# Kernel tuning notes

Hardware: AMD Instinct MI355X
Metric: run time of the kernel (lower is better)

Reference implementation:

```python
import jax, jax.numpy as jnp
import numpy as np
from jax import lax

B, P, E, H, A, V, T = 128, 196, 512, 512, 256, 30000, 21


def setup_inputs() -> dict:
    key = jax.random.key(0)
    ks = jax.random.split(key, 16)
    s = 0.02
    return {
        "encoder_out": jax.random.normal(ks[0], (B, P, E), jnp.float32),
        "captions": jax.random.randint(ks[1], (B, T), 0, V),
        "emb": jax.random.normal(ks[2], (V, E), jnp.float32) * s,
        "W_enc_att": jax.random.normal(ks[3], (E, A), jnp.float32) * s,
        "b_enc_att": jnp.zeros((A,), jnp.float32),
        "W_dec_att": jax.random.normal(ks[4], (H, A), jnp.float32) * s,
        "b_dec_att": jnp.zeros((A,), jnp.float32),
        "w_full_att": jax.random.normal(ks[5], (A,), jnp.float32) * s,
        "b_full_att": jnp.zeros((), jnp.float32),
        "W_ih": jax.random.normal(ks[6], (4 * H, 2 * E), jnp.float32) * s,
        "b_ih": jnp.zeros((4 * H,), jnp.float32),
        "W_hh": jax.random.normal(ks[7], (4 * H, H), jnp.float32) * s,
        "b_hh": jnp.zeros((4 * H,), jnp.float32),
        "W_fc": jax.random.normal(ks[8], (V, H), jnp.float32) * s,
        "b_fc": jnp.zeros((V,), jnp.float32),
    }


def reference(encoder_out, captions, emb, W_enc_att, b_enc_att, W_dec_att, b_dec_att,
              w_full_att, b_full_att, W_ih, b_ih, W_hh, b_hh, W_fc, b_fc):
    # embeddings of captions[:, :-1] -> (B, T-1, E)
    x_emb = emb[captions[:, :-1]]
    # precompute encoder attention projection once (same math, hoisted)
    enc_proj = encoder_out @ W_enc_att + b_enc_att  # (B, P, A)
    h0 = jnp.zeros((encoder_out.shape[0], W_hh.shape[1]), encoder_out.dtype)
    c0 = jnp.zeros_like(h0)

    def step(carry, xt):
        h, c = carry
        # Bahdanau attention: full_att(relu(enc_att + dec_att(h)))
        att = jax.nn.relu(enc_proj + (h @ W_dec_att + b_dec_att)[:, None, :])  # (B,P,A)
        e = att @ w_full_att + b_full_att  # (B, P)
        alpha = jax.nn.softmax(e, axis=1)
        context = jnp.einsum('bp,bpe->be', alpha, encoder_out)  # (B, E)
        x = jnp.concatenate([xt, context], axis=1)  # (B, 2E)
        gates = x @ W_ih.T + b_ih + h @ W_hh.T + b_hh  # (B, 4H)
        i, f, g, o = jnp.split(gates, 4, axis=1)  # PyTorch LSTMCell order
        c_new = jax.nn.sigmoid(f) * c + jax.nn.sigmoid(i) * jnp.tanh(g)
        h_new = jax.nn.sigmoid(o) * jnp.tanh(c_new)
        # dropout is identity in eval/reference mode
        out = h_new @ W_fc.T + b_fc  # (B, V)
        return (h_new, c_new), out

    _, outs = lax.scan(step, (h0, c0), jnp.swapaxes(x_emb, 0, 1))  # (T-1, B, V)
    return jnp.swapaxes(outs, 0, 1)  # (B, T-1, V)
```

## Files before the change

kernel.cpp:

```cpp
#include <hip/hip_runtime.h>
#include <stdint.h>

#define BSZ   128
#define PDIM  196
#define EDIM  512
#define HDIM  512
#define ADIM  256
#define VDIM  30000
#define VPAD  30080
#define NSTEP 20
#define KCAT  1536
#define NGATE 2048
#define KSPLIT 8

typedef __attribute__((ext_vector_type(8))) short short8;
typedef __attribute__((ext_vector_type(4))) float f32x4;

__device__ __forceinline__ unsigned short f2b(float f) {
  union { float f; uint32_t u; } v; v.f = f;
  uint32_t r = v.u + 0x7fffu + ((v.u >> 16) & 1u);
  return (unsigned short)(r >> 16);
}
__device__ __forceinline__ float b2f(unsigned short u) {
  union { uint32_t u; float f; } v; v.u = ((uint32_t)u) << 16;
  return v.f;
}

__device__ __forceinline__ void async16(const void* g, void* l) {
  __builtin_amdgcn_global_load_lds(
      (const __attribute__((address_space(1))) void*)g,
      (__attribute__((address_space(3))) void*)l, 16, 0, 0);
}


__global__ void k_cast_f32_bf16(const float* __restrict__ src,
                                unsigned short* __restrict__ dst, int n4) {
  int i = blockIdx.x * 256 + threadIdx.x;
  if (i < n4) {
    float4 v = ((const float4*)src)[i];
    ushort4 o; o.x = f2b(v.x); o.y = f2b(v.y); o.z = f2b(v.z); o.w = f2b(v.w);
    ((ushort4*)dst)[i] = o;
  }
}

__global__ void k_build_wenc_t(const float* __restrict__ W,
                               unsigned short* __restrict__ WT) {
  int i = blockIdx.x * 256 + threadIdx.x;
  if (i < ADIM * EDIM) {
    int a = i >> 9, k = i & 511;
    WT[i] = f2b(W[k * ADIM + a]);
  }
}

__global__ void k_build_wcat(const float* __restrict__ Wih,
                             const float* __restrict__ Whh,
                             unsigned short* __restrict__ Wcat) {
  int i = blockIdx.x * 256 + threadIdx.x;
  if (i < NGATE * KCAT) {
    int n = i / KCAT, k = i - n * KCAT;
    float v = (k < 1024) ? Wih[n * 1024 + k] : Whh[n * 512 + (k - 1024)];
    Wcat[i] = f2b(v);
  }
}

__global__ void k_build_wfc(const float* __restrict__ Wfc,
                            unsigned short* __restrict__ Wp) {
  int i = blockIdx.x * 256 + threadIdx.x;
  if (i < VPAD * 512) {
    int n = i >> 9, k = i & 511;
    Wp[i] = (n < VDIM) ? f2b(Wfc[n * 512 + k]) : (unsigned short)0;
  }
}

__global__ void k_build_xc(const int* __restrict__ cap,
                           const float* __restrict__ emb,
                           unsigned short* __restrict__ XC) {
  int i = blockIdx.x * 256 + threadIdx.x;
  if (i < NSTEP * BSZ * EDIM) {
    int t = i / (BSZ * EDIM);
    int r = i - t * (BSZ * EDIM);
    int b = r >> 9, k = r & 511;
    int tok = cap[b * 21 + t];
    XC[((size_t)(t * BSZ + b)) * KCAT + k] = f2b(emb[(size_t)tok * EDIM + k]);
  }
}

__global__ void k_init_state(float* __restrict__ hc, float* __restrict__ cc,
                             unsigned short* __restrict__ XC) {
  int i = blockIdx.x * 256 + threadIdx.x;
  if (i < BSZ * HDIM) {
    hc[i] = 0.f; cc[i] = 0.f;
    int b = i >> 9, k = i & 511;
    XC[(size_t)b * KCAT + 1024 + k] = 0;
  }
}


template <bool OUT_BF16>
__global__ __launch_bounds__(256) void gemm_bt(
    const unsigned short* __restrict__ A, int ldaB,
    const unsigned short* __restrict__ Bm, int ldbB,
    void* __restrict__ C, int ldc, int Nreal,
    const float* __restrict__ bias, int kt, int kchunkB, size_t zstride) {
  __shared__ short As[128 * 32];
  __shared__ short Bs[128 * 32];
  const int tid = threadIdx.x;
  const int w = tid >> 6, lane = tid & 63;
  const int m0 = blockIdx.y * 128, n0 = blockIdx.x * 128;
  const int z = blockIdx.z;

  const char* Ab = (const char*)A + (size_t)z * kchunkB;
  const char* Bb = (const char*)Bm + (size_t)z * kchunkB;

  const int q0 = w, q1 = w + 4;
  const int rr = lane >> 2;
  const int cbyte = (lane & 3) * 16;
  const char* gA0 = Ab + (size_t)(m0 + q0 * 16 + rr) * ldaB + cbyte;
  const char* gA1 = Ab + (size_t)(m0 + q1 * 16 + rr) * ldaB + cbyte;
  const char* gB0 = Bb + (size_t)(n0 + q0 * 16 + rr) * ldbB + cbyte;
  const char* gB1 = Bb + (size_t)(n0 + q1 * 16 + rr) * ldbB + cbyte;
  short* lA0 = &As[q0 * 512]; short* lA1 = &As[q1 * 512];
  short* lB0 = &Bs[q0 * 512]; short* lB1 = &Bs[q1 * 512];

  const int wm = w >> 1, wn = w & 1;
  const int fr = lane & 15, ko = (lane >> 4) * 8;

  f32x4 acc[4][4] = {};

  for (int kb = 0; kb < kt; ++kb) {
    const int kB = kb * 64;
    async16(gA0 + kB, lA0); async16(gA1 + kB, lA1);
    async16(gB0 + kB, lB0); async16(gB1 + kB, lB1);
    __syncthreads();
    short8 af[4], bfr[4];
#pragma unroll
    for (int i = 0; i < 4; ++i)
      af[i] = *(const short8*)&As[(wm * 64 + i * 16 + fr) * 32 + ko];
#pragma unroll
    for (int j = 0; j < 4; ++j)
      bfr[j] = *(const short8*)&Bs[(wn * 64 + j * 16 + fr) * 32 + ko];
#pragma unroll
    for (int i = 0; i < 4; ++i)
#pragma unroll
      for (int j = 0; j < 4; ++j)
        acc[i][j] = __builtin_amdgcn_mfma_f32_16x16x32_bf16(af[i], bfr[j], acc[i][j], 0, 0, 0);
    __syncthreads();
  }

  const int r4 = (lane >> 4) * 4;
  float* Cf = (float*)C + (size_t)z * zstride;
  unsigned short* Cb = (unsigned short*)C;
#pragma unroll
  for (int i = 0; i < 4; ++i) {
#pragma unroll
    for (int j = 0; j < 4; ++j) {
      int cc = n0 + wn * 64 + j * 16 + fr;
      if (cc < Nreal) {
        float bv = bias ? bias[cc] : 0.f;
        int r0 = m0 + wm * 64 + i * 16 + r4;
#pragma unroll
        for (int r = 0; r < 4; ++r) {
          float v = acc[i][j][r] + bv;
          if (OUT_BF16) Cb[(size_t)(r0 + r) * ldc + cc] = f2b(v);
          else          Cf[(size_t)(r0 + r) * ldc + cc] = v;
        }
      }
    }
  }
}


__global__ __launch_bounds__(512) void k_attention(
    const float* __restrict__ h, const float* __restrict__ Wd,
    const float* __restrict__ bd, const float* __restrict__ wfull,
    const float* __restrict__ bfull,
    const unsigned short* __restrict__ EncP,
    const unsigned short* __restrict__ EncB,
    unsigned short* __restrict__ XCt)
{
  __shared__ float hsh[512];
  __shared__ float hpp[512];
  __shared__ float hp[256];
  __shared__ float wsh[256];
  __shared__ float ebuf[200];
  __shared__ float sred[8];
  __shared__ float sM, sS;

  const int tid = threadIdx.x;
  const int b = blockIdx.x;
  const int w = tid >> 6, lane = tid & 63;

  hsh[tid] = h[b * 512 + tid];
  if (tid < 256) wsh[tid] = wfull[tid];
  __syncthreads();

  {
    const int a = tid & 255, half = tid >> 8;
    const float* wc = Wd + a;
    const int k0 = half * 256;
    float s0 = 0, s1 = 0, s2 = 0, s3 = 0;
    for (int k = k0; k < k0 + 256; k += 4) {
      s0 += hsh[k]     * wc[(k)     * 256];
      s1 += hsh[k + 1] * wc[(k + 1) * 256];
      s2 += hsh[k + 2] * wc[(k + 2) * 256];
      s3 += hsh[k + 3] * wc[(k + 3) * 256];
    }
    hpp[tid] = (s0 + s1) + (s2 + s3);
  }
  __syncthreads();
  if (tid < 256) hp[tid] = hpp[tid] + hpp[tid + 256] + bd[tid];
  __syncthreads();

  const float bf0 = bfull[0];
  for (int p = w; p < PDIM; p += 8) {
    const unsigned short* row = EncP + ((size_t)(b * PDIM + p)) * 256;
    float s = 0.f;
#pragma unroll
    for (int jj = 0; jj < 4; ++jj) {
      int a = lane + jj * 64;
      float v = b2f(row[a]) + hp[a];
      s += fmaxf(v, 0.f) * wsh[a];
    }
#pragma unroll
    for (int off = 32; off; off >>= 1) s += __shfl_down(s, off, 64);
    if (lane == 0) ebuf[p] = s + bf0;
  }
  __syncthreads();

  float m = -1e30f;
  for (int p = tid; p < PDIM; p += 512) m = fmaxf(m, ebuf[p]);
#pragma unroll
  for (int off = 32; off; off >>= 1) m = fmaxf(m, __shfl_down(m, off, 64));
  if (lane == 0) sred[w] = m;
  __syncthreads();
  if (tid == 0) {
    float mm = sred[0];
#pragma unroll
    for (int i = 1; i < 8; ++i) mm = fmaxf(mm, sred[i]);
    sM = mm;
  }
  __syncthreads();
  const float M = sM;
  float ps = 0.f;
  for (int p = tid; p < PDIM; p += 512) {
    float v = __expf(ebuf[p] - M); ebuf[p] = v; ps += v;
  }
#pragma unroll
  for (int off = 32; off; off >>= 1) ps += __shfl_down(ps, off, 64);
  if (lane == 0) sred[w] = ps;
  __syncthreads();
  if (tid == 0) {
    float ss = 0.f;
#pragma unroll
    for (int i = 0; i < 8; ++i) ss += sred[i];
    sS = 1.f / ss;
  }
  __syncthreads();
  const float inv = sS;

  {
    const unsigned short* eb = EncB + (size_t)b * PDIM * 512;
    float c0 = 0.f;
    for (int p = 0; p < PDIM; ++p) c0 += ebuf[p] * b2f(eb[p * 512 + tid]);
    XCt[(size_t)b * KCAT + 512 + tid] = f2b(c0 * inv);
  }
}


__global__ __launch_bounds__(256) void k_cell(
    const float* __restrict__ Gpart,
    const float* __restrict__ bih, const float* __restrict__ bhh,
    float* __restrict__ hc, float* __restrict__ cc,
    unsigned short* __restrict__ Hall, unsigned short* __restrict__ XCnext, int t) {
  int i = blockIdx.x * 256 + threadIdx.x;
  int b = i >> 9, k = i & 511;
  float gI = bih[k] + bhh[k];
  float gF = bih[512 + k] + bhh[512 + k];
  float gG = bih[1024 + k] + bhh[1024 + k];
  float gO = bih[1536 + k] + bhh[1536 + k];
  const float* P = Gpart + (size_t)b * NGATE;
#pragma unroll
  for (int z = 0; z < KSPLIT; ++z) {
    const float* Pz = P + (size_t)z * BSZ * NGATE;
    gI += Pz[k]; gF += Pz[512 + k]; gG += Pz[1024 + k]; gO += Pz[1536 + k];
  }
  float cv = cc[i];
  float ig = 1.f / (1.f + __expf(-gI));
  float fg = 1.f / (1.f + __expf(-gF));
  float gg = tanhf(gG);
  float og = 1.f / (1.f + __expf(-gO));
  float cn = fg * cv + ig * gg;
  float hn = og * tanhf(cn);
  cc[i] = cn; hc[i] = hn;
  Hall[((size_t)b * NSTEP + t) * 512 + k] = f2b(hn);
  if (t < NSTEP - 1) XCnext[(size_t)b * KCAT + 1024 + k] = f2b(hn);
}


extern "C" void kernel_launch(void* const* d_in, const int* in_sizes, int n_in,
                              void* d_out, int out_size, void* d_ws, size_t ws_size,
                              hipStream_t stream) {
  const float* enc   = (const float*)d_in[0];
  const int*   cap   = (const int*)d_in[1];
  const float* emb   = (const float*)d_in[2];
  const float* Wenc  = (const float*)d_in[3];
  const float* benc  = (const float*)d_in[4];
  const float* Wdec  = (const float*)d_in[5];
  const float* bdec  = (const float*)d_in[6];
  const float* wfull = (const float*)d_in[7];
  const float* bfull = (const float*)d_in[8];
  const float* Wih   = (const float*)d_in[9];
  const float* bih   = (const float*)d_in[10];
  const float* Whh   = (const float*)d_in[11];
  const float* bhh   = (const float*)d_in[12];
  const float* Wfc   = (const float*)d_in[13];
  const float* bfc   = (const float*)d_in[14];
  float* out = (float*)d_out;

  char* ws = (char*)d_ws;
  size_t off = 0;
  auto alloc = [&](size_t bytes) {
    char* p = ws + off;
    off += (bytes + 255) & ~(size_t)255;
    return p;
  };
  unsigned short* Wcat  = (unsigned short*)alloc((size_t)NGATE * KCAT * 2);
  unsigned short* Wfcb  = (unsigned short*)alloc((size_t)VPAD * 512 * 2);
  unsigned short* WencT = (unsigned short*)alloc((size_t)ADIM * EDIM * 2);
  unsigned short* EncB  = (unsigned short*)alloc((size_t)BSZ * PDIM * EDIM * 2);
  unsigned short* EncP  = (unsigned short*)alloc((size_t)BSZ * PDIM * ADIM * 2);
  unsigned short* XC    = (unsigned short*)alloc((size_t)NSTEP * BSZ * KCAT * 2);
  float* Gpart          = (float*)alloc((size_t)KSPLIT * BSZ * NGATE * 4);
  float* hc             = (float*)alloc((size_t)BSZ * HDIM * 4);
  float* ccst           = (float*)alloc((size_t)BSZ * HDIM * 4);
  unsigned short* Hall  = (unsigned short*)alloc((size_t)NSTEP * BSZ * HDIM * 2);
  (void)ws_size; (void)in_sizes; (void)n_in; (void)out_size;

  {
    int n4 = BSZ * PDIM * EDIM / 4;
    k_cast_f32_bf16<<<(n4 + 255) / 256, 256, 0, stream>>>(enc, EncB, n4);
  }
  k_build_wenc_t<<<(ADIM * EDIM + 255) / 256, 256, 0, stream>>>(Wenc, WencT);
  k_build_wcat<<<(NGATE * KCAT + 255) / 256, 256, 0, stream>>>(Wih, Whh, Wcat);
  k_build_wfc<<<(VPAD * 512 + 255) / 256, 256, 0, stream>>>(Wfc, Wfcb);
  k_build_xc<<<(NSTEP * BSZ * EDIM + 255) / 256, 256, 0, stream>>>(cap, emb, XC);
  k_init_state<<<(BSZ * HDIM + 255) / 256, 256, 0, stream>>>(hc, ccst, XC);

  gemm_bt<true><<<dim3(2, 196, 1), 256, 0, stream>>>(
      EncB, EDIM * 2, WencT, EDIM * 2, EncP, ADIM, ADIM, benc, 16, 0, 0);

  for (int t = 0; t < NSTEP; ++t) {
    unsigned short* XCt = XC + (size_t)t * BSZ * KCAT;
    k_attention<<<128, 512, 0, stream>>>(hc, Wdec, bdec, wfull, bfull, EncP, EncB, XCt);
    gemm_bt<false><<<dim3(NGATE / 128, 1, KSPLIT), 256, 0, stream>>>(
        XCt, KCAT * 2, Wcat, KCAT * 2, Gpart, NGATE, NGATE, nullptr,
        (KCAT / KSPLIT) / 32, (KCAT / KSPLIT) * 2, (size_t)BSZ * NGATE);
    unsigned short* XCn = XC + (size_t)((t + 1 < NSTEP) ? (t + 1) : 0) * BSZ * KCAT;
    k_cell<<<BSZ * HDIM / 256, 256, 0, stream>>>(Gpart, bih, bhh, hc, ccst, Hall, XCn, t);
  }

  gemm_bt<false><<<dim3(VPAD / 128, NSTEP * BSZ / 128, 1), 256, 0, stream>>>(
      Hall, HDIM * 2, Wfcb, HDIM * 2, out, VDIM, VDIM, bfc, 16, 0, 0);
}
```

Baseline: 1.508 ms.

## Hoist embedding gate GEMM out of recurrence and fuse LSTM cell with attention

The embedding part of the input-gate GEMM (x_emb @ W_ih[:, :512]) is now computed once for all timesteps as one large GEMM before the loop, so each step's split-K GEMM only covers the 1024 context+hidden columns. The LSTM cell update and the next step's attention are fused into one 512-thread-per-batch kernel, cutting one launch per step and the round trip of h through global memory. The context accumulation is also unrolled with four partial sums. In exchange it adds an fp32 XW buffer that every step must read, and the attention now runs with only 128 blocks after the cell update.

```diff
diff --git a/kernel.cpp b/kernel.cpp
--- a/kernel.cpp
+++ b/kernel.cpp
@@ -10,6 +10,7 @@
 #define VPAD  30080
 #define NSTEP 20
 #define KCAT  1536
+#define KSTEP 1024
 #define NGATE 2048
 #define KSPLIT 8
 
@@ -72,16 +73,16 @@
   }
 }
 
-__global__ void k_build_xc(const int* __restrict__ cap,
-                           const float* __restrict__ emb,
-                           unsigned short* __restrict__ XC) {
+__global__ void k_build_xemb(const int* __restrict__ cap,
+                             const float* __restrict__ emb,
+                             unsigned short* __restrict__ X) {
   int i = blockIdx.x * 256 + threadIdx.x;
   if (i < NSTEP * BSZ * EDIM) {
     int t = i / (BSZ * EDIM);
     int r = i - t * (BSZ * EDIM);
     int b = r >> 9, k = r & 511;
     int tok = cap[b * 21 + t];
-    XC[((size_t)(t * BSZ + b)) * KCAT + k] = f2b(emb[(size_t)tok * EDIM + k]);
+    X[((size_t)(t * BSZ + b)) * EDIM + k] = f2b(emb[(size_t)tok * EDIM + k]);
   }
 }
 
@@ -91,7 +92,7 @@
   if (i < BSZ * HDIM) {
     hc[i] = 0.f; cc[i] = 0.f;
     int b = i >> 9, k = i & 511;
-    XC[(size_t)b * KCAT + 1024 + k] = 0;
+    XC[(size_t)b * KSTEP + 512 + k] = 0;
   }
 }
 
@@ -259,41 +260,147 @@
   const float inv = sS;
 
   {
-    const unsigned short* eb = EncB + (size_t)b * PDIM * 512;
-    float c0 = 0.f;
-    for (int p = 0; p < PDIM; ++p) c0 += ebuf[p] * b2f(eb[p * 512 + tid]);
-    XCt[(size_t)b * KCAT + 512 + tid] = f2b(c0 * inv);
-  }
-}
-
-
-__global__ __launch_bounds__(256) void k_cell(
+    const unsigned short* eb = EncB + (size_t)b * PDIM * 512 + tid;
+    float c0 = 0.f, c1 = 0.f, c2 = 0.f, c3 = 0.f;
+    for (int p = 0; p < PDIM; p += 4) {
+      c0 += ebuf[p]     * b2f(eb[(p)     * 512]);
+      c1 += ebuf[p + 1] * b2f(eb[(p + 1) * 512]);
+      c2 += ebuf[p + 2] * b2f(eb[(p + 2) * 512]);
+      c3 += ebuf[p + 3] * b2f(eb[(p + 3) * 512]);
+    }
+    XCt[(size_t)b * KSTEP + tid] = f2b(((c0 + c1) + (c2 + c3)) * inv);
+  }
+}
+
+
+__global__ __launch_bounds__(512) void k_cell_attn(
     const float* __restrict__ Gpart,
+    const float* __restrict__ XW,
     const float* __restrict__ bih, const float* __restrict__ bhh,
-    float* __restrict__ hc, float* __restrict__ cc,
-    unsigned short* __restrict__ Hall, unsigned short* __restrict__ XCnext, int t) {
-  int i = blockIdx.x * 256 + threadIdx.x;
-  int b = i >> 9, k = i & 511;
-  float gI = bih[k] + bhh[k];
-  float gF = bih[512 + k] + bhh[512 + k];
-  float gG = bih[1024 + k] + bhh[1024 + k];
-  float gO = bih[1536 + k] + bhh[1536 + k];
-  const float* P = Gpart + (size_t)b * NGATE;
-#pragma unroll
-  for (int z = 0; z < KSPLIT; ++z) {
-    const float* Pz = P + (size_t)z * BSZ * NGATE;
-    gI += Pz[k]; gF += Pz[512 + k]; gG += Pz[1024 + k]; gO += Pz[1536 + k];
-  }
-  float cv = cc[i];
-  float ig = 1.f / (1.f + __expf(-gI));
-  float fg = 1.f / (1.f + __expf(-gF));
-  float gg = tanhf(gG);
-  float og = 1.f / (1.f + __expf(-gO));
-  float cn = fg * cv + ig * gg;
-  float hn = og * tanhf(cn);
-  cc[i] = cn; hc[i] = hn;
-  Hall[((size_t)b * NSTEP + t) * 512 + k] = f2b(hn);
-  if (t < NSTEP - 1) XCnext[(size_t)b * KCAT + 1024 + k] = f2b(hn);
+    float* __restrict__ cc, unsigned short* __restrict__ Hall,
+    const float* __restrict__ Wd, const float* __restrict__ bd,
+    const float* __restrict__ wfull, const float* __restrict__ bfull,
+    const unsigned short* __restrict__ EncP,
+    const unsigned short* __restrict__ EncB,
+    unsigned short* __restrict__ XCnext, int t) {
+  __shared__ float hsh[512];
+  __shared__ float hpp[512];
+  __shared__ float hp[256];
+  __shared__ float wsh[256];
+  __shared__ float ebuf[200];
+  __shared__ float sred[8];
+  __shared__ float sM, sS;
+
+  const int tid = threadIdx.x;
+  const int b = blockIdx.x;
+  const int w = tid >> 6, lane = tid & 63;
+
+  if (tid < 256) wsh[tid] = wfull[tid];
+
+  {
+    const int k = tid;
+    const float* xw = XW + ((size_t)(t * BSZ + b)) * NGATE;
+    float gI = bih[k]        + bhh[k]        + xw[k];
+    float gF = bih[512 + k]  + bhh[512 + k]  + xw[512 + k];
+    float gG = bih[1024 + k] + bhh[1024 + k] + xw[1024 + k];
+    float gO = bih[1536 + k] + bhh[1536 + k] + xw[1536 + k];
+    const float* P = Gpart + (size_t)b * NGATE + k;
+#pragma unroll
+    for (int z = 0; z < KSPLIT; ++z) {
+      const float* Pz = P + (size_t)z * BSZ * NGATE;
+      gI += Pz[0]; gF += Pz[512]; gG += Pz[1024]; gO += Pz[1536];
+    }
+    float cv = cc[b * 512 + k];
+    float ig = 1.f / (1.f + __expf(-gI));
+    float fg = 1.f / (1.f + __expf(-gF));
+    float gg = tanhf(gG);
+    float og = 1.f / (1.f + __expf(-gO));
+    float cn = fg * cv + ig * gg;
+    float hn = og * tanhf(cn);
+    cc[b * 512 + k] = cn;
+    Hall[((size_t)b * NSTEP + t) * 512 + k] = f2b(hn);
+    hsh[k] = hn;
+    if (t < NSTEP - 1) XCnext[(size_t)b * KSTEP + 512 + k] = f2b(hn);
+  }
+  __syncthreads();
+  if (t >= NSTEP - 1) return;
+
+
+  {
+    const int a = tid & 255, half = tid >> 8;
+    const float* wc = Wd + a;
+    const int k0 = half * 256;
+    float s0 = 0, s1 = 0, s2 = 0, s3 = 0;
+    for (int k = k0; k < k0 + 256; k += 4) {
+      s0 += hsh[k]     * wc[(k)     * 256];
+      s1 += hsh[k + 1] * wc[(k + 1) * 256];
+      s2 += hsh[k + 2] * wc[(k + 2) * 256];
+      s3 += hsh[k + 3] * wc[(k + 3) * 256];
+    }
+    hpp[tid] = (s0 + s1) + (s2 + s3);
+  }
+  __syncthreads();
+  if (tid < 256) hp[tid] = hpp[tid] + hpp[tid + 256] + bd[tid];
+  __syncthreads();
+
+  const float bf0 = bfull[0];
+  for (int p = w; p < PDIM; p += 8) {
+    const unsigned short* row = EncP + ((size_t)(b * PDIM + p)) * 256;
+    float s = 0.f;
+#pragma unroll
+    for (int jj = 0; jj < 4; ++jj) {
+      int a = lane + jj * 64;
+      float v = b2f(row[a]) + hp[a];
+      s += fmaxf(v, 0.f) * wsh[a];
+    }
+#pragma unroll
+    for (int off = 32; off; off >>= 1) s += __shfl_down(s, off, 64);
+    if (lane == 0) ebuf[p] = s + bf0;
+  }
+  __syncthreads();
+
+  float m = -1e30f;
+  for (int p = tid; p < PDIM; p += 512) m = fmaxf(m, ebuf[p]);
+#pragma unroll
+  for (int off = 32; off; off >>= 1) m = fmaxf(m, __shfl_down(m, off, 64));
+  if (lane == 0) sred[w] = m;
+  __syncthreads();
+  if (tid == 0) {
+    float mm = sred[0];
+#pragma unroll
+    for (int i = 1; i < 8; ++i) mm = fmaxf(mm, sred[i]);
+    sM = mm;
+  }
+  __syncthreads();
+  const float M = sM;
+  float ps = 0.f;
+  for (int p = tid; p < PDIM; p += 512) {
+    float v = __expf(ebuf[p] - M); ebuf[p] = v; ps += v;
+  }
+#pragma unroll
+  for (int off = 32; off; off >>= 1) ps += __shfl_down(ps, off, 64);
+  if (lane == 0) sred[w] = ps;
+  __syncthreads();
+  if (tid == 0) {
+    float ss = 0.f;
+#pragma unroll
+    for (int i = 0; i < 8; ++i) ss += sred[i];
+    sS = 1.f / ss;
+  }
+  __syncthreads();
+  const float inv = sS;
+
+  {
+    const unsigned short* eb = EncB + (size_t)b * PDIM * 512 + tid;
+    float c0 = 0.f, c1 = 0.f, c2 = 0.f, c3 = 0.f;
+    for (int p = 0; p < PDIM; p += 4) {
+      c0 += ebuf[p]     * b2f(eb[(p)     * 512]);
+      c1 += ebuf[p + 1] * b2f(eb[(p + 1) * 512]);
+      c2 += ebuf[p + 2] * b2f(eb[(p + 2) * 512]);
+      c3 += ebuf[p + 3] * b2f(eb[(p + 3) * 512]);
+    }
+    XCnext[(size_t)b * KSTEP + tid] = f2b(((c0 + c1) + (c2 + c3)) * inv);
+  }
 }
 
 
@@ -329,7 +436,9 @@
   unsigned short* WencT = (unsigned short*)alloc((size_t)ADIM * EDIM * 2);
   unsigned short* EncB  = (unsigned short*)alloc((size_t)BSZ * PDIM * EDIM * 2);
   unsigned short* EncP  = (unsigned short*)alloc((size_t)BSZ * PDIM * ADIM * 2);
-  unsigned short* XC    = (unsigned short*)alloc((size_t)NSTEP * BSZ * KCAT * 2);
+  unsigned short* XC    = (unsigned short*)alloc((size_t)NSTEP * BSZ * KSTEP * 2);
+  unsigned short* Xemb  = (unsigned short*)alloc((size_t)NSTEP * BSZ * EDIM * 2);
+  float* XW             = (float*)alloc((size_t)NSTEP * BSZ * NGATE * 4);
   float* Gpart          = (float*)alloc((size_t)KSPLIT * BSZ * NGATE * 4);
   float* hc             = (float*)alloc((size_t)BSZ * HDIM * 4);
   float* ccst           = (float*)alloc((size_t)BSZ * HDIM * 4);
@@ -343,20 +452,25 @@
   k_build_wenc_t<<<(ADIM * EDIM + 255) / 256, 256, 0, stream>>>(Wenc, WencT);
   k_build_wcat<<<(NGATE * KCAT + 255) / 256, 256, 0, stream>>>(Wih, Whh, Wcat);
   k_build_wfc<<<(VPAD * 512 + 255) / 256, 256, 0, stream>>>(Wfc, Wfcb);
-  k_build_xc<<<(NSTEP * BSZ * EDIM + 255) / 256, 256, 0, stream>>>(cap, emb, XC);
+  k_build_xemb<<<(NSTEP * BSZ * EDIM + 255) / 256, 256, 0, stream>>>(cap, emb, Xemb);
   k_init_state<<<(BSZ * HDIM + 255) / 256, 256, 0, stream>>>(hc, ccst, XC);
 
   gemm_bt<true><<<dim3(2, 196, 1), 256, 0, stream>>>(
       EncB, EDIM * 2, WencT, EDIM * 2, EncP, ADIM, ADIM, benc, 16, 0, 0);
 
+  gemm_bt<false><<<dim3(NGATE / 128, NSTEP * BSZ / 128, 1), 256, 0, stream>>>(
+      Xemb, EDIM * 2, Wcat, KCAT * 2, XW, NGATE, NGATE, nullptr, 16, 0, 0);
+
+  k_attention<<<128, 512, 0, stream>>>(hc, Wdec, bdec, wfull, bfull, EncP, EncB, XC);
+
   for (int t = 0; t < NSTEP; ++t) {
-    unsigned short* XCt = XC + (size_t)t * BSZ * KCAT;
-    k_attention<<<128, 512, 0, stream>>>(hc, Wdec, bdec, wfull, bfull, EncP, EncB, XCt);
+    unsigned short* XCt = XC + (size_t)t * BSZ * KSTEP;
     gemm_bt<false><<<dim3(NGATE / 128, 1, KSPLIT), 256, 0, stream>>>(
-        XCt, KCAT * 2, Wcat, KCAT * 2, Gpart, NGATE, NGATE, nullptr,
-        (KCAT / KSPLIT) / 32, (KCAT / KSPLIT) * 2, (size_t)BSZ * NGATE);
-    unsigned short* XCn = XC + (size_t)((t + 1 < NSTEP) ? (t + 1) : 0) * BSZ * KCAT;
-    k_cell<<<BSZ * HDIM / 256, 256, 0, stream>>>(Gpart, bih, bhh, hc, ccst, Hall, XCn, t);
+        XCt, KSTEP * 2, Wcat + 512, KCAT * 2, Gpart, NGATE, NGATE, nullptr,
+        (KSTEP / KSPLIT) / 32, (KSTEP / KSPLIT) * 2, (size_t)BSZ * NGATE);
+    unsigned short* XCn = XC + (size_t)((t + 1 < NSTEP) ? (t + 1) : 0) * BSZ * KSTEP;
+    k_cell_attn<<<128, 512, 0, stream>>>(Gpart, XW, bih, bhh, ccst, Hall,
+                                         Wdec, bdec, wfull, bfull, EncP, EncB, XCn, t);
   }
 
   gemm_bt<false><<<dim3(VPAD / 128, NSTEP * BSZ / 128, 1), 256, 0, stream>>>(
```

After: 1.444 ms. -4.2%, faster.

## Fuse recurrent loop into persistent kernel with grid barriers and hoisted embedding GEMM

Applied to the files above, without the earlier changes.

Replaces the 60 per-step launches (attention, split-K gate GEMM, cell) with a single persistent 128-block kernel that synchronises through an atomic grid barrier. The input-embedding half of the gate GEMM is hoisted out of the loop into one batched GEMM over all steps, so each step only multiplies the context and hidden parts. The decoder-attention projection now uses bf16 weights, and the score and context loops are vectorised. The aim is to remove launch overhead and redundant per-step work. In exchange it relies on all 128 blocks being co-resident for the spin barrier and adds bf16 rounding to W_dec.

```diff
diff --git a/kernel.cpp b/kernel.cpp
--- a/kernel.cpp
+++ b/kernel.cpp
@@ -10,6 +10,7 @@
 #define VPAD  30080
 #define NSTEP 20
 #define KCAT  1536
+#define KSTEP 1024
 #define NGATE 2048
 #define KSPLIT 8
 
@@ -25,6 +26,12 @@
   union { uint32_t u; float f; } v; v.u = ((uint32_t)u) << 16;
   return v.f;
 }
+__device__ __forceinline__ float ulo(uint32_t u) {
+  union { uint32_t u; float f; } v; v.u = u << 16; return v.f;
+}
+__device__ __forceinline__ float uhi(uint32_t u) {
+  union { uint32_t u; float f; } v; v.u = u & 0xffff0000u; return v.f;
+}
 
 __device__ __forceinline__ void async16(const void* g, void* l) {
   __builtin_amdgcn_global_load_lds(
@@ -32,6 +39,17 @@
       (__attribute__((address_space(3))) void*)l, 16, 0, 0);
 }
 
+__device__ __forceinline__ void gsync(unsigned* bar, unsigned target) {
+  __threadfence();
+  __syncthreads();
+  if (threadIdx.x == 0) {
+    __hip_atomic_fetch_add(bar, 1u, __ATOMIC_RELEASE, __HIP_MEMORY_SCOPE_AGENT);
+    while (__hip_atomic_load(bar, __ATOMIC_ACQUIRE, __HIP_MEMORY_SCOPE_AGENT) < target)
+      __builtin_amdgcn_s_sleep(1);
+  }
+  __syncthreads();
+}
+
 
 __global__ void k_cast_f32_bf16(const float* __restrict__ src,
                                 unsigned short* __restrict__ dst, int n4) {
@@ -72,26 +90,34 @@
   }
 }
 
-__global__ void k_build_xc(const int* __restrict__ cap,
-                           const float* __restrict__ emb,
-                           unsigned short* __restrict__ XC) {
+__global__ void k_build_xemb(const int* __restrict__ cap,
+                             const float* __restrict__ emb,
+                             unsigned short* __restrict__ X) {
   int i = blockIdx.x * 256 + threadIdx.x;
   if (i < NSTEP * BSZ * EDIM) {
     int t = i / (BSZ * EDIM);
     int r = i - t * (BSZ * EDIM);
     int b = r >> 9, k = r & 511;
     int tok = cap[b * 21 + t];
-    XC[((size_t)(t * BSZ + b)) * KCAT + k] = f2b(emb[(size_t)tok * EDIM + k]);
-  }
-}
-
-__global__ void k_init_state(float* __restrict__ hc, float* __restrict__ cc,
-                             unsigned short* __restrict__ XC) {
-  int i = blockIdx.x * 256 + threadIdx.x;
+    X[((size_t)(t * BSZ + b)) * EDIM + k] = f2b(emb[(size_t)tok * EDIM + k]);
+  }
+}
+
+__global__ void k_build_wdb(const float* __restrict__ Wd,
+                            unsigned short* __restrict__ o) {
+  int i = blockIdx.x * 256 + threadIdx.x;
+  if (i < HDIM * ADIM) o[i] = f2b(Wd[i]);
+}
+
+__global__ void k_init_state(float* __restrict__ cc,
+                             unsigned short* __restrict__ XC,
+                             unsigned* __restrict__ bar) {
+  int i = blockIdx.x * 256 + threadIdx.x;
+  if (i == 0) *bar = 0u;
   if (i < BSZ * HDIM) {
-    hc[i] = 0.f; cc[i] = 0.f;
+    cc[i] = 0.f;
     int b = i >> 9, k = i & 511;
-    XC[(size_t)b * KCAT + 1024 + k] = 0;
+    XC[(size_t)b * KSTEP + 512 + k] = 0;
   }
 }
 
@@ -170,130 +196,239 @@
 }
 
 
-__global__ __launch_bounds__(512) void k_attention(
-    const float* __restrict__ h, const float* __restrict__ Wd,
-    const float* __restrict__ bd, const float* __restrict__ wfull,
-    const float* __restrict__ bfull,
+__device__ __forceinline__ void attn_234(
+    int b, int tid, int w, int lane, float bf0,
     const unsigned short* __restrict__ EncP,
     const unsigned short* __restrict__ EncB,
-    unsigned short* __restrict__ XCt)
+    const float* hp, const float* wsh,
+    float* ebuf, float* red, float* sred, float* sMS,
+    unsigned short* __restrict__ XCdst)
 {
+  const float hpr0 = hp[lane * 4],     hpr1 = hp[lane * 4 + 1];
+  const float hpr2 = hp[lane * 4 + 2], hpr3 = hp[lane * 4 + 3];
+  const float wsr0 = wsh[lane * 4],     wsr1 = wsh[lane * 4 + 1];
+  const float wsr2 = wsh[lane * 4 + 2], wsr3 = wsh[lane * 4 + 3];
+  for (int pb = w * 4; pb < PDIM; pb += 32) {
+    float s0 = 0.f, s1 = 0.f, s2 = 0.f, s3 = 0.f;
+#pragma unroll
+    for (int q = 0; q < 4; ++q) {
+      int p = pb + q;
+      if (p < PDIM) {
+        short4 v = *((const short4*)(EncP + (size_t)(b * PDIM + p) * 256) + lane);
+        float t0 = fmaxf(b2f((unsigned short)v.x) + hpr0, 0.f) * wsr0;
+        float t1 = fmaxf(b2f((unsigned short)v.y) + hpr1, 0.f) * wsr1;
+        float t2 = fmaxf(b2f((unsigned short)v.z) + hpr2, 0.f) * wsr2;
+        float t3 = fmaxf(b2f((unsigned short)v.w) + hpr3, 0.f) * wsr3;
+        float sq = (t0 + t1) + (t2 + t3);
+        if (q == 0) s0 = sq; else if (q == 1) s1 = sq;
+        else if (q == 2) s2 = sq; else s3 = sq;
+      }
+    }
+#pragma unroll
+    for (int off = 32; off; off >>= 1) {
+      s0 += __shfl_xor(s0, off, 64);
+      s1 += __shfl_xor(s1, off, 64);
+      s2 += __shfl_xor(s2, off, 64);
+      s3 += __shfl_xor(s3, off, 64);
+    }
+    if (lane < 4) {
+      int p = pb + lane;
+      float v = (lane == 0) ? s0 : (lane == 1) ? s1 : (lane == 2) ? s2 : s3;
+      if (p < PDIM) ebuf[p] = v + bf0;
+    }
+  }
+  __syncthreads();
+
+  float m = -1e30f;
+  for (int p = tid; p < PDIM; p += 512) m = fmaxf(m, ebuf[p]);
+#pragma unroll
+  for (int off = 32; off; off >>= 1) m = fmaxf(m, __shfl_down(m, off, 64));
+  if (lane == 0) sred[w] = m;
+  __syncthreads();
+  if (tid == 0) {
+    float mm = sred[0];
+#pragma unroll
+    for (int i = 1; i < 8; ++i) mm = fmaxf(mm, sred[i]);
+    sMS[0] = mm;
+  }
+  __syncthreads();
+  const float M = sMS[0];
+  float ps = 0.f;
+  for (int p = tid; p < PDIM; p += 512) {
+    float v = __expf(ebuf[p] - M); ebuf[p] = v; ps += v;
+  }
+#pragma unroll
+  for (int off = 32; off; off >>= 1) ps += __shfl_down(ps, off, 64);
+  if (lane == 0) sred[w] = ps;
+  __syncthreads();
+  if (tid == 0) {
+    float ss = 0.f;
+#pragma unroll
+    for (int i = 0; i < 8; ++i) ss += sred[i];
+    sMS[1] = 1.f / ss;
+  }
+  __syncthreads();
+  const float inv = sMS[1];
+
+  {
+    const int c2 = tid & 255, ph = tid >> 8;
+    const uint32_t* eb = (const uint32_t*)(EncB + (size_t)b * PDIM * 512) + c2;
+    float c0 = 0.f, c1 = 0.f, d0 = 0.f, d1 = 0.f;
+    const int p0 = ph * 98;
+    for (int p = p0; p < p0 + 98; p += 2) {
+      float a0 = ebuf[p];     uint32_t u  = eb[(size_t)p * 256];
+      c0 = fmaf(a0, ulo(u),  c0); c1 = fmaf(a0, uhi(u),  c1);
+      float a1 = ebuf[p + 1]; uint32_t u2 = eb[(size_t)(p + 1) * 256];
+      d0 = fmaf(a1, ulo(u2), d0); d1 = fmaf(a1, uhi(u2), d1);
+    }
+    red[ph * 512 + c2 * 2]     = c0 + d0;
+    red[ph * 512 + c2 * 2 + 1] = c1 + d1;
+  }
+  __syncthreads();
+  float v = (red[tid] + red[512 + tid]) * inv;
+  XCdst[(size_t)b * KSTEP + tid] = f2b(v);
+}
+
+
+__global__ __launch_bounds__(512, 1) void k_loop(
+    unsigned short* __restrict__ XC,
+    const unsigned short* __restrict__ Wcat,
+    float* __restrict__ Gpart,
+    const float* __restrict__ XW,
+    const float* __restrict__ bih, const float* __restrict__ bhh,
+    float* __restrict__ ccst, unsigned short* __restrict__ Hall,
+    const unsigned short* __restrict__ Wdb,
+    const float* __restrict__ bd,
+    const float* __restrict__ wfull, const float* __restrict__ bfull,
+    const unsigned short* __restrict__ EncP,
+    const unsigned short* __restrict__ EncB,
+    unsigned* __restrict__ bar)
+{
+  __shared__ short As[128 * 32];
+  __shared__ short Bs[128 * 32];
   __shared__ float hsh[512];
-  __shared__ float hpp[512];
+  __shared__ float red[1024];
   __shared__ float hp[256];
   __shared__ float wsh[256];
   __shared__ float ebuf[200];
   __shared__ float sred[8];
-  __shared__ float sM, sS;
-
-  const int tid = threadIdx.x;
-  const int b = blockIdx.x;
+  __shared__ float sMS[2];
+
+  const int tid = threadIdx.x, blk = blockIdx.x;
   const int w = tid >> 6, lane = tid & 63;
-
-  hsh[tid] = h[b * 512 + tid];
-  if (tid < 256) wsh[tid] = wfull[tid];
-  __syncthreads();
-
-  {
-    const int a = tid & 255, half = tid >> 8;
-    const float* wc = Wd + a;
-    const int k0 = half * 256;
-    float s0 = 0, s1 = 0, s2 = 0, s3 = 0;
-    for (int k = k0; k < k0 + 256; k += 4) {
-      s0 += hsh[k]     * wc[(k)     * 256];
-      s1 += hsh[k + 1] * wc[(k + 1) * 256];
-      s2 += hsh[k + 2] * wc[(k + 2) * 256];
-      s3 += hsh[k + 3] * wc[(k + 3) * 256];
-    }
-    hpp[tid] = (s0 + s1) + (s2 + s3);
-  }
-  __syncthreads();
-  if (tid < 256) hp[tid] = hpp[tid] + hpp[tid + 256] + bd[tid];
-  __syncthreads();
-
+  const int b = blk;
+  const int gn0 = (blk >> 3) * 128, gz = blk & 7;
   const float bf0 = bfull[0];
-  for (int p = w; p < PDIM; p += 8) {
-    const unsigned short* row = EncP + ((size_t)(b * PDIM + p)) * 256;
-    float s = 0.f;
-#pragma unroll
-    for (int jj = 0; jj < 4; ++jj) {
-      int a = lane + jj * 64;
-      float v = b2f(row[a]) + hp[a];
-      s += fmaxf(v, 0.f) * wsh[a];
-    }
-#pragma unroll
-    for (int off = 32; off; off >>= 1) s += __shfl_down(s, off, 64);
-    if (lane == 0) ebuf[p] = s + bf0;
-  }
-  __syncthreads();
-
-  float m = -1e30f;
-  for (int p = tid; p < PDIM; p += 512) m = fmaxf(m, ebuf[p]);
-#pragma unroll
-  for (int off = 32; off; off >>= 1) m = fmaxf(m, __shfl_down(m, off, 64));
-  if (lane == 0) sred[w] = m;
-  __syncthreads();
-  if (tid == 0) {
-    float mm = sred[0];
-#pragma unroll
-    for (int i = 1; i < 8; ++i) mm = fmaxf(mm, sred[i]);
-    sM = mm;
-  }
-  __syncthreads();
-  const float M = sM;
-  float ps = 0.f;
-  for (int p = tid; p < PDIM; p += 512) {
-    float v = __expf(ebuf[p] - M); ebuf[p] = v; ps += v;
-  }
-#pragma unroll
-  for (int off = 32; off; off >>= 1) ps += __shfl_down(ps, off, 64);
-  if (lane == 0) sred[w] = ps;
-  __syncthreads();
-  if (tid == 0) {
-    float ss = 0.f;
-#pragma unroll
-    for (int i = 0; i < 8; ++i) ss += sred[i];
-    sS = 1.f / ss;
-  }
-  __syncthreads();
-  const float inv = sS;
-
-  {
-    const unsigned short* eb = EncB + (size_t)b * PDIM * 512;
-    float c0 = 0.f;
-    for (int p = 0; p < PDIM; ++p) c0 += ebuf[p] * b2f(eb[p * 512 + tid]);
-    XCt[(size_t)b * KCAT + 512 + tid] = f2b(c0 * inv);
-  }
-}
-
-
-__global__ __launch_bounds__(256) void k_cell(
-    const float* __restrict__ Gpart,
-    const float* __restrict__ bih, const float* __restrict__ bhh,
-    float* __restrict__ hc, float* __restrict__ cc,
-    unsigned short* __restrict__ Hall, unsigned short* __restrict__ XCnext, int t) {
-  int i = blockIdx.x * 256 + threadIdx.x;
-  int b = i >> 9, k = i & 511;
-  float gI = bih[k] + bhh[k];
-  float gF = bih[512 + k] + bhh[512 + k];
-  float gG = bih[1024 + k] + bhh[1024 + k];
-  float gO = bih[1536 + k] + bhh[1536 + k];
-  const float* P = Gpart + (size_t)b * NGATE;
-#pragma unroll
-  for (int z = 0; z < KSPLIT; ++z) {
-    const float* Pz = P + (size_t)z * BSZ * NGATE;
-    gI += Pz[k]; gF += Pz[512 + k]; gG += Pz[1024 + k]; gO += Pz[1536 + k];
-  }
-  float cv = cc[i];
-  float ig = 1.f / (1.f + __expf(-gI));
-  float fg = 1.f / (1.f + __expf(-gF));
-  float gg = tanhf(gG);
-  float og = 1.f / (1.f + __expf(-gO));
-  float cn = fg * cv + ig * gg;
-  float hn = og * tanhf(cn);
-  cc[i] = cn; hc[i] = hn;
-  Hall[((size_t)b * NSTEP + t) * 512 + k] = f2b(hn);
-  if (t < NSTEP - 1) XCnext[(size_t)b * KCAT + 1024 + k] = f2b(hn);
+  unsigned bc = 0;
+
+  if (tid < 256) { wsh[tid] = wfull[tid]; hp[tid] = bd[tid]; }
+  __syncthreads();
+
+  attn_234(b, tid, w, lane, bf0, EncP, EncB, hp, wsh, ebuf, red, sred, sMS, XC);
+
+  for (int t = 0; t < NSTEP; ++t) {
+    gsync(bar, bc += 128);
+
+    {
+      const char* Ab = (const char*)(XC + (size_t)t * BSZ * KSTEP) + gz * 256;
+      const char* Bb = (const char*)Wcat + 1024 + gz * 256;
+      const int rr = lane >> 2, cb = (lane & 3) * 16;
+      const char* gA = Ab + (size_t)(w * 16 + rr) * (KSTEP * 2) + cb;
+      const char* gB = Bb + (size_t)(gn0 + w * 16 + rr) * (KCAT * 2) + cb;
+      short* lA = &As[w * 512];
+      short* lB = &Bs[w * 512];
+      const int wm = w >> 2, wn = w & 3;
+      const int fr = lane & 15, ko = (lane >> 4) * 8;
+      f32x4 acc[4][2] = {};
+#pragma unroll
+      for (int kb = 0; kb < 4; ++kb) {
+        async16(gA + kb * 64, lA);
+        async16(gB + kb * 64, lB);
+        __syncthreads();
+        short8 af[4], bfr[2];
+#pragma unroll
+        for (int i = 0; i < 4; ++i)
+          af[i] = *(const short8*)&As[(wm * 64 + i * 16 + fr) * 32 + ko];
+#pragma unroll
+        for (int j = 0; j < 2; ++j)
+          bfr[j] = *(const short8*)&Bs[(wn * 32 + j * 16 + fr) * 32 + ko];
+#pragma unroll
+        for (int i = 0; i < 4; ++i)
+#pragma unroll
+          for (int j = 0; j < 2; ++j)
+            acc[i][j] = __builtin_amdgcn_mfma_f32_16x16x32_bf16(af[i], bfr[j], acc[i][j], 0, 0, 0);
+        __syncthreads();
+      }
+      float* Cz = Gpart + (size_t)gz * BSZ * NGATE;
+      const int r4 = (lane >> 4) * 4;
+#pragma unroll
+      for (int i = 0; i < 4; ++i)
+#pragma unroll
+        for (int j = 0; j < 2; ++j) {
+          int ccol = gn0 + wn * 32 + j * 16 + fr;
+          int r0 = wm * 64 + i * 16 + r4;
+#pragma unroll
+          for (int r = 0; r < 4; ++r)
+            Cz[(size_t)(r0 + r) * NGATE + ccol] = acc[i][j][r];
+        }
+    }
+
+    gsync(bar, bc += 128);
+
+    unsigned short* XCn = XC + (size_t)(t + 1) * BSZ * KSTEP;
+    {
+      const int k = tid;
+      const float* xw = XW + ((size_t)t * BSZ + b) * NGATE;
+      float gI = bih[k]        + bhh[k]        + xw[k];
+      float gF = bih[512 + k]  + bhh[512 + k]  + xw[512 + k];
+      float gG = bih[1024 + k] + bhh[1024 + k] + xw[1024 + k];
+      float gO = bih[1536 + k] + bhh[1536 + k] + xw[1536 + k];
+      const float* P = Gpart + (size_t)b * NGATE + k;
+#pragma unroll
+      for (int z = 0; z < KSPLIT; ++z) {
+        const float* Pz = P + (size_t)z * BSZ * NGATE;
+        gI += Pz[0]; gF += Pz[512]; gG += Pz[1024]; gO += Pz[1536];
+      }
+      float cv = ccst[b * 512 + k];
+      float ig = 1.f / (1.f + __expf(-gI));
+      float fg = 1.f / (1.f + __expf(-gF));
+      float gg = tanhf(gG);
+      float og = 1.f / (1.f + __expf(-gO));
+      float cn = fg * cv + ig * gg;
+      float hn = og * tanhf(cn);
+      ccst[b * 512 + k] = cn;
+      hsh[k] = hn;
+      Hall[((size_t)b * NSTEP + t) * 512 + k] = f2b(hn);
+      if (t < NSTEP - 1) XCn[(size_t)b * KSTEP + 512 + k] = f2b(hn);
+    }
+    __syncthreads();
+
+    if (t < NSTEP - 1) {
+      {
+        const int p2 = tid & 127, kq = tid >> 7;
+        const uint32_t* wrow = (const uint32_t*)Wdb + p2;
+        float s0 = 0.f, s1 = 0.f, s2 = 0.f, s3 = 0.f;
+        const int k0 = kq * 128;
+#pragma unroll 4
+        for (int k = k0; k < k0 + 128; k += 2) {
+          uint32_t u = wrow[(size_t)k * 128];
+          float hv = hsh[k];
+          s0 = fmaf(hv, ulo(u), s0); s1 = fmaf(hv, uhi(u), s1);
+          uint32_t u2 = wrow[(size_t)(k + 1) * 128];
+          float hv2 = hsh[k + 1];
+          s2 = fmaf(hv2, ulo(u2), s2); s3 = fmaf(hv2, uhi(u2), s3);
+        }
+        red[kq * 256 + p2 * 2]     = s0 + s2;
+        red[kq * 256 + p2 * 2 + 1] = s1 + s3;
+      }
+      __syncthreads();
+      if (tid < 256)
+        hp[tid] = bd[tid] + ((red[tid] + red[256 + tid]) + (red[512 + tid] + red[768 + tid]));
+      __syncthreads();
+
+      attn_234(b, tid, w, lane, bf0, EncP, EncB, hp, wsh, ebuf, red, sred, sMS, XCn);
+    }
+  }
 }
 
 
@@ -329,11 +464,14 @@
   unsigned short* WencT = (unsigned short*)alloc((size_t)ADIM * EDIM * 2);
   unsigned short* EncB  = (unsigned short*)alloc((size_t)BSZ * PDIM * EDIM * 2);
   unsigned short* EncP  = (unsigned short*)alloc((size_t)BSZ * PDIM * ADIM * 2);
-  unsigned short* XC    = (unsigned short*)alloc((size_t)NSTEP * BSZ * KCAT * 2);
+  unsigned short* XC    = (unsigned short*)alloc((size_t)NSTEP * BSZ * KSTEP * 2);
+  unsigned short* Xemb  = (unsigned short*)alloc((size_t)NSTEP * BSZ * EDIM * 2);
+  float* XW             = (float*)alloc((size_t)NSTEP * BSZ * NGATE * 4);
   float* Gpart          = (float*)alloc((size_t)KSPLIT * BSZ * NGATE * 4);
-  float* hc             = (float*)alloc((size_t)BSZ * HDIM * 4);
   float* ccst           = (float*)alloc((size_t)BSZ * HDIM * 4);
   unsigned short* Hall  = (unsigned short*)alloc((size_t)NSTEP * BSZ * HDIM * 2);
+  unsigned short* Wdb   = (unsigned short*)alloc((size_t)HDIM * ADIM * 2);
+  unsigned* bar         = (unsigned*)alloc(256);
   (void)ws_size; (void)in_sizes; (void)n_in; (void)out_size;
 
   {
@@ -343,21 +481,18 @@
   k_build_wenc_t<<<(ADIM * EDIM + 255) / 256, 256, 0, stream>>>(Wenc, WencT);
   k_build_wcat<<<(NGATE * KCAT + 255) / 256, 256, 0, stream>>>(Wih, Whh, Wcat);
   k_build_wfc<<<(VPAD * 512 + 255) / 256, 256, 0, stream>>>(Wfc, Wfcb);
-  k_build_xc<<<(NSTEP * BSZ * EDIM + 255) / 256, 256, 0, stream>>>(cap, emb, XC);
-  k_init_state<<<(BSZ * HDIM + 255) / 256, 256, 0, stream>>>(hc, ccst, XC);
+  k_build_xemb<<<(NSTEP * BSZ * EDIM + 255) / 256, 256, 0, stream>>>(cap, emb, Xemb);
+  k_build_wdb<<<(HDIM * ADIM + 255) / 256, 256, 0, stream>>>(Wdec, Wdb);
+  k_init_state<<<(BSZ * HDIM + 255) / 256, 256, 0, stream>>>(ccst, XC, bar);
 
   gemm_bt<true><<<dim3(2, 196, 1), 256, 0, stream>>>(
       EncB, EDIM * 2, WencT, EDIM * 2, EncP, ADIM, ADIM, benc, 16, 0, 0);
 
-  for (int t = 0; t < NSTEP; ++t) {
-    unsigned short* XCt = XC + (size_t)t * BSZ * KCAT;
-    k_attention<<<128, 512, 0, stream>>>(hc, Wdec, bdec, wfull, bfull, EncP, EncB, XCt);
-    gemm_bt<false><<<dim3(NGATE / 128, 1, KSPLIT), 256, 0, stream>>>(
-        XCt, KCAT * 2, Wcat, KCAT * 2, Gpart, NGATE, NGATE, nullptr,
-        (KCAT / KSPLIT) / 32, (KCAT / KSPLIT) * 2, (size_t)BSZ * NGATE);
-    unsigned short* XCn = XC + (size_t)((t + 1 < NSTEP) ? (t + 1) : 0) * BSZ * KCAT;
-    k_cell<<<BSZ * HDIM / 256, 256, 0, stream>>>(Gpart, bih, bhh, hc, ccst, Hall, XCn, t);
-  }
+  gemm_bt<false><<<dim3(NGATE / 128, NSTEP * BSZ / 128, 1), 256, 0, stream>>>(
+      Xemb, EDIM * 2, Wcat, KCAT * 2, XW, NGATE, NGATE, nullptr, 16, 0, 0);
+
+  k_loop<<<128, 512, 0, stream>>>(XC, Wcat, Gpart, XW, bih, bhh, ccst, Hall,
+                                  Wdb, bdec, wfull, bfull, EncP, EncB, bar);
 
   gemm_bt<false><<<dim3(VPAD / 128, NSTEP * BSZ / 128, 1), 256, 0, stream>>>(
       Hall, HDIM * 2, Wfcb, HDIM * 2, out, VDIM, VDIM, bfc, 16, 0, 0);
```

Result: slower. 3.200 ms (+112.1%).
